# Performance work log

Hardware: AMD Instinct MI355X
Metric: run time of the kernel (lower is better)

## Reference

```python
import jax, jax.numpy as jnp
import numpy as np

B, S, E, H = 4, 1024, 1024, 16
HD = E // H

def setup_inputs() -> dict:
    key = jax.random.key(0)
    ks = jax.random.split(key, 12)
    std = 1.0 / np.sqrt(E)
    inp = {
        "query": jax.random.normal(ks[0], (B, S, E), jnp.float32),
        "key_t": jax.random.normal(ks[1], (B, S, E), jnp.float32),
        "value": jax.random.normal(ks[2], (B, S, E), jnp.float32),
        # causal mask, broadcastable to (B, H, S, S); 0 => masked
        "mask": jnp.tril(jnp.ones((S, S), jnp.int32))[None, None],
        "Wq": jax.random.normal(ks[3], (E, E), jnp.float32) * std,
        "bq": jnp.zeros((E,), jnp.float32),
        "Wk": jax.random.normal(ks[4], (E, E), jnp.float32) * std,
        "bk": jnp.zeros((E,), jnp.float32),
        "Wv": jax.random.normal(ks[5], (E, E), jnp.float32) * std,
        "bv": jnp.zeros((E,), jnp.float32),
        "Wo": jax.random.normal(ks[6], (E, E), jnp.float32) * std,
        "bo": jnp.zeros((E,), jnp.float32),
    }
    return inp

def reference(query, key_t, value, mask, Wq, bq, Wk, bk, Wv, bv, Wo, bo):
    scale = jnp.asarray(np.sqrt(HD), query.dtype)
    # projections (torch Linear: x @ W.T + b), split into heads -> (B, H, S, HD)
    def split_heads(x):
        return x.reshape(B, S, H, HD).transpose(0, 2, 1, 3)
    q = split_heads(query @ Wq.T + bq)
    k = split_heads(key_t @ Wk.T + bk)
    v = split_heads(value @ Wv.T + bv)
    scores = jnp.einsum("bhqd,bhkd->bhqk", q, k) / scale  # (B,H,S,S)
    scores = jnp.where(mask == 0, jnp.asarray(-jnp.inf, scores.dtype), scores)
    attn = jax.nn.softmax(scores, axis=-1)
    # dropout is identity in eval / p=0
    out = jnp.einsum("bhqk,bhkd->bhqd", attn, v)
    out = out.transpose(0, 2, 1, 3).reshape(B, S, E)
    out = out @ Wo.T + bo
    return out, attn
```

## Files before the change

### kernel.cpp

```cpp
#include <hip/hip_runtime.h>
#include <hip/hip_bf16.h>


typedef short bf16x8 __attribute__((ext_vector_type(8)));
typedef float f32x4 __attribute__((ext_vector_type(4)));

__device__ __forceinline__ unsigned short f2bf(float f) {
  union { float f; unsigned u; } v; v.f = f;
  unsigned r = v.u + 0x7FFF + ((v.u >> 16) & 1);
  return (unsigned short)(r >> 16);
}

__device__ __forceinline__ void gload16(const unsigned short* g, unsigned short* l) {
  __builtin_amdgcn_global_load_lds(
      (const __attribute__((address_space(1))) unsigned int*)g,
      (__attribute__((address_space(3))) unsigned int*)l, 16, 0, 0);
}

__global__ __launch_bounds__(256) void cast3_k(
    const float* __restrict__ a, const float* __restrict__ b,
    const float* __restrict__ c,
    unsigned short* __restrict__ oa, unsigned short* __restrict__ ob,
    unsigned short* __restrict__ oc) {
  const float* in = blockIdx.y == 0 ? a : blockIdx.y == 1 ? b : c;
  unsigned short* out = blockIdx.y == 0 ? oa : blockIdx.y == 1 ? ob : oc;
  int i = (blockIdx.x * 256 + threadIdx.x) * 8;
  float4 x = *(const float4*)(in + i);
  float4 y = *(const float4*)(in + i + 4);
  unsigned short t[8] = { f2bf(x.x), f2bf(x.y), f2bf(x.z), f2bf(x.w),
                          f2bf(y.x), f2bf(y.y), f2bf(y.z), f2bf(y.w) };
  *(bf16x8*)(out + i) = *(bf16x8*)t;
}

__global__ __launch_bounds__(256) void cast4_k(
    const float* __restrict__ a, const float* __restrict__ b,
    const float* __restrict__ c, const float* __restrict__ d,
    unsigned short* __restrict__ oa, unsigned short* __restrict__ ob,
    unsigned short* __restrict__ oc, unsigned short* __restrict__ od) {
  const float* in = blockIdx.y == 0 ? a : blockIdx.y == 1 ? b : blockIdx.y == 2 ? c : d;
  unsigned short* out = blockIdx.y == 0 ? oa : blockIdx.y == 1 ? ob : blockIdx.y == 2 ? oc : od;
  int i = (blockIdx.x * 256 + threadIdx.x) * 8;
  float4 x = *(const float4*)(in + i);
  float4 y = *(const float4*)(in + i + 4);
  unsigned short t[8] = { f2bf(x.x), f2bf(x.y), f2bf(x.z), f2bf(x.w),
                          f2bf(y.x), f2bf(y.y), f2bf(y.z), f2bf(y.w) };
  *(bf16x8*)(out + i) = *(bf16x8*)t;
}

__device__ __forceinline__ void gemm_core(
    const unsigned short* __restrict__ A, const unsigned short* __restrict__ W,
    int m0, int n0, int K, unsigned short* As, unsigned short* Bs, f32x4 acc[4][4])
{
  const int tid = threadIdx.x;
  const int w = tid >> 6, lane = tid & 63, quad = lane >> 4, lc = lane & 15;
  const int wm = (w >> 1) * 64, wn = (w & 1) * 64;
  const int lrow = lane >> 3, lg = lane & 7;

  for (int kb = 0; kb < K; kb += 64) {
#pragma unroll
    for (int t = 0; t < 4; t++) {
      int row = w * 32 + t * 8 + lrow;
      int gsw = lg ^ (row & 7);
      gload16(&A[(size_t)(m0 + row) * K + kb + gsw * 8], &As[(w * 32 + t * 8) * 64]);
      gload16(&W[(size_t)(n0 + row) * K + kb + gsw * 8], &Bs[(w * 32 + t * 8) * 64]);
    }
    __syncthreads();
#pragma unroll
    for (int kk = 0; kk < 2; kk++) {
      bf16x8 af[4], bfr[4];
#pragma unroll
      for (int i = 0; i < 4; i++) {
        int ra = wm + i * 16 + lc;
        af[i] = *(const bf16x8*)&As[ra * 64 + (((kk * 4 + quad) ^ (ra & 7)) * 8)];
      }
#pragma unroll
      for (int j = 0; j < 4; j++) {
        int rb = wn + j * 16 + lc;
        bfr[j] = *(const bf16x8*)&Bs[rb * 64 + (((kk * 4 + quad) ^ (rb & 7)) * 8)];
      }
#pragma unroll
      for (int i = 0; i < 4; i++)
#pragma unroll
        for (int j = 0; j < 4; j++)
          acc[i][j] = __builtin_amdgcn_mfma_f32_16x16x32_bf16(af[i], bfr[j], acc[i][j], 0, 0, 0);
    }
    __syncthreads();
  }
}

__global__ __launch_bounds__(256) void gemm_qkv(
    const unsigned short* __restrict__ Xq, const unsigned short* __restrict__ Xk,
    const unsigned short* __restrict__ Xv,
    const unsigned short* __restrict__ Wq, const unsigned short* __restrict__ Wk,
    const unsigned short* __restrict__ Wv,
    const float* __restrict__ bq, const float* __restrict__ bk, const float* __restrict__ bv,
    unsigned short* __restrict__ Qb, unsigned short* __restrict__ Kb,
    unsigned short* __restrict__ Vt)
{
  __shared__ __align__(16) unsigned short S[128 * 136];
  unsigned short* As = S;
  unsigned short* Bs = S + 128 * 64;
  const int z = blockIdx.z;
  const unsigned short* A = z == 0 ? Xq : z == 1 ? Xk : Xv;
  const unsigned short* W = z == 0 ? Wq : z == 1 ? Wk : Wv;
  const float* bias = z == 0 ? bq : z == 1 ? bk : bv;
  unsigned short* outRM = z == 0 ? Qb : Kb;
  const int m0 = blockIdx.x * 128, n0 = blockIdx.y * 128;
  const int tid = threadIdx.x;
  const int w = tid >> 6, lane = tid & 63, quad = lane >> 4, lc = lane & 15;
  const int wm = (w >> 1) * 64, wn = (w & 1) * 64;

  f32x4 acc[4][4] = {};
  gemm_core(A, W, m0, n0, 1024, As, Bs, acc);

  if (z < 2) {
#pragma unroll
    for (int j = 0; j < 4; j++) {
      int col = n0 + wn + j * 16 + lc;
      float bvl = bias[col];
#pragma unroll
      for (int i = 0; i < 4; i++)
#pragma unroll
        for (int r = 0; r < 4; r++) {
          int row = m0 + wm + i * 16 + quad * 4 + r;
          outRM[(size_t)row * 1024 + col] = f2bf(acc[i][j][r] + bvl);
        }
    }
  } else {
    unsigned short* T = S;
#pragma unroll
    for (int j = 0; j < 4; j++) {
      int col = wn + j * 16 + lc;
      float bvl = bias[n0 + col];
#pragma unroll
      for (int i = 0; i < 4; i++)
#pragma unroll
        for (int r = 0; r < 4; r++) {
          int row = wm + i * 16 + quad * 4 + r;
          T[col * 136 + (((row >> 3) ^ (col & 7)) << 3) + (row & 7)] =
              f2bf(acc[i][j][r] + bvl);
        }
    }
    __syncthreads();
    const int b_ = m0 >> 10, sb = m0 & 1023;
#pragma unroll
    for (int it = 0; it < 8; it++) {
      int cl = w * 32 + it * 4 + (lane >> 4);
      int sg = lane & 15;
      int colg = n0 + cl;
      *(bf16x8*)&Vt[((size_t)((b_ * 16 + (colg >> 6)) * 64 + (colg & 63))) * 1024 + sb + sg * 8] =
          *(const bf16x8*)&T[cl * 136 + ((sg ^ (cl & 7)) << 3)];
    }
  }
}

__global__ __launch_bounds__(256) void gemm_out(
    const unsigned short* __restrict__ A, const unsigned short* __restrict__ W,
    const float* __restrict__ bias, float* __restrict__ outf)
{
  __shared__ __align__(16) unsigned short As[128 * 64];
  __shared__ __align__(16) unsigned short Bs[128 * 64];
  const int m0 = blockIdx.x * 128, n0 = blockIdx.y * 128;
  const int tid = threadIdx.x;
  const int w = tid >> 6, lane = tid & 63, quad = lane >> 4, lc = lane & 15;
  const int wm = (w >> 1) * 64, wn = (w & 1) * 64;

  f32x4 acc[4][4] = {};
  gemm_core(A, W, m0, n0, 1024, As, Bs, acc);

#pragma unroll
  for (int j = 0; j < 4; j++) {
    int col = n0 + wn + j * 16 + lc;
    float bvl = bias[col];
#pragma unroll
    for (int i = 0; i < 4; i++)
#pragma unroll
      for (int r = 0; r < 4; r++) {
        int row = m0 + wm + i * 16 + quad * 4 + r;
        outf[(size_t)row * 1024 + col] = acc[i][j][r] + bvl;
      }
  }
}

__global__ __launch_bounds__(256) void attn_fused(
    const unsigned short* __restrict__ Qb,
    const unsigned short* __restrict__ Kb,
    const unsigned short* __restrict__ Vt,
    float* __restrict__ attn,
    unsigned short* __restrict__ O)
{
  __shared__ __align__(16) unsigned short Ks[64 * 64];
  __shared__ __align__(16) unsigned short Vs[64 * 64];
  __shared__ __align__(16) unsigned short Pl[4][16][40];
  __shared__ __align__(16) float          Ps[4][16][36];
  const int bh = blockIdx.x, b = bh >> 4, h = bh & 15;
  const int by = (int)gridDim.y - 1 - (int)blockIdx.y;
  const int q0 = by * 64;
  const int tid = threadIdx.x;
  const int w = tid >> 6, lane = tid & 63, quad = lane >> 4, lc = lane & 15;
  const int g0 = q0 + w * 16;
  const int kt_d = g0 >> 4;
  const int nch = by + 1;
  const int sr = lane >> 3, sg = lane & 7;

  const unsigned short* qp = Qb + ((size_t)(b * 1024 + g0 + lc)) * 1024 + h * 64 + quad * 8;
  bf16x8 a0 = *(const bf16x8*)qp;
  bf16x8 a1 = *(const bf16x8*)(qp + 32);

  float m_[4] = { -1e30f, -1e30f, -1e30f, -1e30f };
  float l_[4] = { 0.f, 0.f, 0.f, 0.f };

  for (int c = 0; c < nch; c++) {
    int kv0 = c * 64;
    {
      int r0 = w * 8 + sr, r1 = 32 + r0;
      gload16(&Kb[((size_t)(b * 1024 + kv0 + r0)) * 1024 + h * 64 + (sg ^ (r0 & 7)) * 8],
              &Ks[(w * 8) * 64]);
      gload16(&Kb[((size_t)(b * 1024 + kv0 + r1)) * 1024 + h * 64 + (sg ^ (r1 & 7)) * 8],
              &Ks[(32 + w * 8) * 64]);
    }
    __syncthreads();
    int tmax = kt_d - c * 4;
    int tlim = tmax < 3 ? tmax : 3;
    for (int t = 0; t <= tlim; t++) {
      int rk = t * 16 + lc;
      const unsigned short* kr = &Ks[rk * 64];
      bf16x8 b0 = *(const bf16x8*)&kr[((quad ^ (rk & 7))) * 8];
      bf16x8 b1 = *(const bf16x8*)&kr[(((quad + 4) ^ (rk & 7))) * 8];
      f32x4 cc = {};
      cc = __builtin_amdgcn_mfma_f32_16x16x32_bf16(a0, b0, cc, 0, 0, 0);
      cc = __builtin_amdgcn_mfma_f32_16x16x32_bf16(a1, b1, cc, 0, 0, 0);
      if (t < tmax) {
#pragma unroll
        for (int r = 0; r < 4; r++) {
          float s = cc[r] * 0.125f;
          float mn = fmaxf(m_[r], s);
          l_[r] = l_[r] * __expf(m_[r] - mn) + __expf(s - mn);
          m_[r] = mn;
        }
      } else {
#pragma unroll
        for (int r = 0; r < 4; r++) {
          int qr = g0 + quad * 4 + r;
          float sv = (kv0 + t * 16 + lc) > qr ? -1e30f : cc[r] * 0.125f;
          float mn = fmaxf(m_[r], sv);
          l_[r] = l_[r] * __expf(m_[r] - mn) + __expf(sv - mn);
          m_[r] = mn;
        }
      }
    }
    __syncthreads();
  }

  float mofs[4];
#pragma unroll
  for (int r = 0; r < 4; r++) {
    float mT = m_[r];
#pragma unroll
    for (int off = 1; off < 16; off <<= 1) mT = fmaxf(mT, __shfl_xor(mT, off));
    float lt = l_[r] * __expf(m_[r] - mT);
#pragma unroll
    for (int off = 1; off < 16; off <<= 1) lt += __shfl_xor(lt, off);
    mofs[r] = mT + __logf(lt);
  }

  float* arow = attn + (size_t)bh * 1024 * 1024;
  f32x4 oacc[4] = {};
  for (int c = 0; c < nch; c++) {
    int kv0 = c * 64;
    {
      int r0 = w * 8 + sr, r1 = 32 + r0;
      gload16(&Kb[((size_t)(b * 1024 + kv0 + r0)) * 1024 + h * 64 + (sg ^ (r0 & 7)) * 8],
              &Ks[(w * 8) * 64]);
      gload16(&Kb[((size_t)(b * 1024 + kv0 + r1)) * 1024 + h * 64 + (sg ^ (r1 & 7)) * 8],
              &Ks[(32 + w * 8) * 64]);
      gload16(&Vt[((size_t)(bh * 64 + r0)) * 1024 + kv0 + (sg ^ (r0 & 7)) * 8],
              &Vs[(w * 8) * 64]);
      gload16(&Vt[((size_t)(bh * 64 + r1)) * 1024 + kv0 + (sg ^ (r1 & 7)) * 8],
              &Vs[(32 + w * 8) * 64]);
    }
    __syncthreads();
    int tmax = kt_d - c * 4;
#pragma unroll
    for (int u = 0; u < 2; u++) {
      if (u * 2 <= tmax) {
#pragma unroll
        for (int t2 = 0; t2 < 2; t2++) {
          int t = u * 2 + t2;
          if (t <= tmax) {
            int rk = t * 16 + lc;
            const unsigned short* kr = &Ks[rk * 64];
            bf16x8 b0 = *(const bf16x8*)&kr[((quad ^ (rk & 7))) * 8];
            bf16x8 b1 = *(const bf16x8*)&kr[(((quad + 4) ^ (rk & 7))) * 8];
            f32x4 cc = {};
            cc = __builtin_amdgcn_mfma_f32_16x16x32_bf16(a0, b0, cc, 0, 0, 0);
            cc = __builtin_amdgcn_mfma_f32_16x16x32_bf16(a1, b1, cc, 0, 0, 0);
#pragma unroll
            for (int r = 0; r < 4; r++) {
              int qr = g0 + quad * 4 + r;
              float p = (kv0 + t * 16 + lc) > qr ? 0.f : __expf(cc[r] * 0.125f - mofs[r]);
              Ps[w][quad * 4 + r][t2 * 16 + lc] = p;
              Pl[w][quad * 4 + r][t2 * 16 + lc] = f2bf(p);
            }
          } else {
#pragma unroll
            for (int r = 0; r < 4; r++) Pl[w][quad * 4 + r][t2 * 16 + lc] = 0;
          }
        }
        bf16x8 pa = *(const bf16x8*)&Pl[w][lc][quad * 8];
#pragma unroll
        for (int j = 0; j < 4; j++) {
          int hd = j * 16 + lc;
          bf16x8 bv = *(const bf16x8*)&Vs[hd * 64 + (((u * 4 + quad) ^ (hd & 7)) * 8)];
          oacc[j] = __builtin_amdgcn_mfma_f32_16x16x32_bf16(pa, bv, oacc[j], 0, 0, 0);
        }
        int nt = tmax - u * 2 + 1; if (nt > 2) nt = 2;
        int srow = lane >> 2, cf = (lane & 3) * 4;
        float* dst = &arow[(size_t)(g0 + srow) * 1024 + kv0 + u * 32];
        *(float4*)(dst + cf) = *(const float4*)&Ps[w][srow][cf];
        if (nt == 2)
          *(float4*)(dst + 16 + cf) = *(const float4*)&Ps[w][srow][16 + cf];
      }
    }
    __syncthreads();
  }

  {
    int rr = lane >> 2, cl = lane & 3;
    float4 z = make_float4(0.f, 0.f, 0.f, 0.f);
    for (int c0 = g0 + 16 + cl * 4; c0 < 1024; c0 += 16)
      *(float4*)&arow[(size_t)(g0 + rr) * 1024 + c0] = z;
  }

  {
    unsigned short* ob = (unsigned short*)&Ps[w][0][0];
#pragma unroll
    for (int j = 0; j < 4; j++)
#pragma unroll
      for (int r = 0; r < 4; r++)
        ob[(quad * 4 + r) * 72 + j * 16 + lc] = f2bf(oacc[j][r]);
#pragma unroll
    for (int it = 0; it < 2; it++) {
      int row = it * 8 + (lane >> 3), off = (lane & 7) * 8;
      *(bf16x8*)&O[((size_t)(b * 1024 + g0 + row)) * 1024 + h * 64 + off] =
          *(const bf16x8*)&ob[row * 72 + off];
    }
  }
}

extern "C" void kernel_launch(void* const* d_in, const int* in_sizes, int n_in,
                              void* d_out, int out_size, void* d_ws, size_t ws_size,
                              hipStream_t stream) {
  const float* query = (const float*)d_in[0];
  const float* key_t = (const float*)d_in[1];
  const float* value = (const float*)d_in[2];
  const float* Wq = (const float*)d_in[4];
  const float* bq = (const float*)d_in[5];
  const float* Wk = (const float*)d_in[6];
  const float* bk = (const float*)d_in[7];
  const float* Wv = (const float*)d_in[8];
  const float* bv = (const float*)d_in[9];
  const float* Wo = (const float*)d_in[10];
  const float* bo = (const float*)d_in[11];

  unsigned short* Xq  = (unsigned short*)d_ws;
  unsigned short* Xk  = Xq  + 4194304;
  unsigned short* Xv  = Xk  + 4194304;
  unsigned short* Wqb = Xv  + 4194304;
  unsigned short* Wkb = Wqb + 1048576;
  unsigned short* Wvb = Wkb + 1048576;
  unsigned short* Wob = Wvb + 1048576;
  unsigned short* Qb  = Wob + 1048576;
  unsigned short* Kb  = Qb  + 4194304;
  unsigned short* Vtb = Kb  + 4194304;
  unsigned short* Ob  = Vtb + 4194304;

  float* outO = (float*)d_out;
  float* attn = outO + 4194304;

  cast3_k<<<dim3(2048, 3), 256, 0, stream>>>(query, key_t, value, Xq, Xk, Xv);
  cast4_k<<<dim3(512, 4), 256, 0, stream>>>(Wq, Wk, Wv, Wo, Wqb, Wkb, Wvb, Wob);

  gemm_qkv<<<dim3(32, 8, 3), 256, 0, stream>>>(Xq, Xk, Xv, Wqb, Wkb, Wvb,
                                               bq, bk, bv, Qb, Kb, Vtb);

  attn_fused<<<dim3(64, 16), 256, 0, stream>>>(Qb, Kb, Vtb, attn, Ob);

  gemm_out<<<dim3(32, 8), 256, 0, stream>>>(Ob, Wob, bo, outO);
}
```

Before: 482.3 us.

## Double-buffer K/V tiles in attention and write attn probabilities from bf16 P

Adds double-buffered K and V shared tiles in both attention passes so the next chunk's global-to-LDS loads are in flight while the current one is computed, with explicit vmcnt waits and raw barriers. Pre-scales Q by 1/8 in bf16 and splits the two MFMA accumulations, so scores no longer need a multiply. Drops the fp32 Ps staging buffer and writes the attn output by widening the bf16 P tile. The attn matrix therefore carries bf16 rounding error, and the hand-placed waitcnt/barrier sequencing is fragile.

Result: no change. 484.3 us (+0.4%).

```diff
diff --git a/kernel.cpp b/kernel.cpp
--- a/kernel.cpp
+++ b/kernel.cpp
@@ -4,11 +4,18 @@
 
 typedef short bf16x8 __attribute__((ext_vector_type(8)));
 typedef float f32x4 __attribute__((ext_vector_type(4)));
+
+#define VMCNT(n) asm volatile("s_waitcnt vmcnt(" #n ")" ::: "memory")
 
 __device__ __forceinline__ unsigned short f2bf(float f) {
   union { float f; unsigned u; } v; v.f = f;
   unsigned r = v.u + 0x7FFF + ((v.u >> 16) & 1);
   return (unsigned short)(r >> 16);
+}
+
+__device__ __forceinline__ float bf2f(unsigned short u) {
+  union { unsigned u; float f; } v; v.u = ((unsigned)u) << 16;
+  return v.f;
 }
 
 __device__ __forceinline__ void gload16(const unsigned short* g, unsigned short* l) {
@@ -189,10 +196,9 @@
     float* __restrict__ attn,
     unsigned short* __restrict__ O)
 {
-  __shared__ __align__(16) unsigned short Ks[64 * 64];
-  __shared__ __align__(16) unsigned short Vs[64 * 64];
+  __shared__ __align__(16) unsigned short Ks[2][64 * 64];
+  __shared__ __align__(16) unsigned short Vs[2][64 * 64];
   __shared__ __align__(16) unsigned short Pl[4][16][40];
-  __shared__ __align__(16) float          Ps[4][16][36];
   const int bh = blockIdx.x, b = bh >> 4, h = bh & 15;
   const int by = (int)gridDim.y - 1 - (int)blockIdx.y;
   const int q0 = by * 64;
@@ -202,38 +208,59 @@
   const int kt_d = g0 >> 4;
   const int nch = by + 1;
   const int sr = lane >> 3, sg = lane & 7;
-
-  const unsigned short* qp = Qb + ((size_t)(b * 1024 + g0 + lc)) * 1024 + h * 64 + quad * 8;
-  bf16x8 a0 = *(const bf16x8*)qp;
-  bf16x8 a1 = *(const bf16x8*)(qp + 32);
+  const int r0_ = w * 8 + sr, r1_ = 32 + r0_;
+
+  bf16x8 a0, a1;
+  {
+    const unsigned short* qp = Qb + ((size_t)(b * 1024 + g0 + lc)) * 1024 + h * 64 + quad * 8;
+    bf16x8 q0v = *(const bf16x8*)qp;
+    bf16x8 q1v = *(const bf16x8*)(qp + 32);
+#pragma unroll
+    for (int i = 0; i < 8; i++) {
+      a0[i] = (short)f2bf(bf2f((unsigned short)q0v[i]) * 0.125f);
+      a1[i] = (short)f2bf(bf2f((unsigned short)q1v[i]) * 0.125f);
+    }
+  }
 
   float m_[4] = { -1e30f, -1e30f, -1e30f, -1e30f };
   float l_[4] = { 0.f, 0.f, 0.f, 0.f };
 
+  {
+    gload16(&Kb[((size_t)(b * 1024 + 0 + r0_)) * 1024 + h * 64 + (sg ^ (r0_ & 7)) * 8],
+            &Ks[0][(w * 8) * 64]);
+    gload16(&Kb[((size_t)(b * 1024 + 0 + r1_)) * 1024 + h * 64 + (sg ^ (r1_ & 7)) * 8],
+            &Ks[0][(32 + w * 8) * 64]);
+  }
   for (int c = 0; c < nch; c++) {
+    const unsigned short* Kc = Ks[c & 1];
     int kv0 = c * 64;
-    {
-      int r0 = w * 8 + sr, r1 = 32 + r0;
-      gload16(&Kb[((size_t)(b * 1024 + kv0 + r0)) * 1024 + h * 64 + (sg ^ (r0 & 7)) * 8],
-              &Ks[(w * 8) * 64]);
-      gload16(&Kb[((size_t)(b * 1024 + kv0 + r1)) * 1024 + h * 64 + (sg ^ (r1 & 7)) * 8],
-              &Ks[(32 + w * 8) * 64]);
-    }
-    __syncthreads();
+    if (c + 1 < nch) {
+      int nv0 = kv0 + 64;
+      unsigned short* Kn = Ks[(c + 1) & 1];
+      gload16(&Kb[((size_t)(b * 1024 + nv0 + r0_)) * 1024 + h * 64 + (sg ^ (r0_ & 7)) * 8],
+              &Kn[(w * 8) * 64]);
+      gload16(&Kb[((size_t)(b * 1024 + nv0 + r1_)) * 1024 + h * 64 + (sg ^ (r1_ & 7)) * 8],
+              &Kn[(32 + w * 8) * 64]);
+      VMCNT(2);
+    } else {
+      VMCNT(0);
+    }
+    __builtin_amdgcn_s_barrier();
+    __builtin_amdgcn_sched_barrier(0);
     int tmax = kt_d - c * 4;
     int tlim = tmax < 3 ? tmax : 3;
     for (int t = 0; t <= tlim; t++) {
       int rk = t * 16 + lc;
-      const unsigned short* kr = &Ks[rk * 64];
+      const unsigned short* kr = &Kc[rk * 64];
       bf16x8 b0 = *(const bf16x8*)&kr[((quad ^ (rk & 7))) * 8];
       bf16x8 b1 = *(const bf16x8*)&kr[(((quad + 4) ^ (rk & 7))) * 8];
-      f32x4 cc = {};
-      cc = __builtin_amdgcn_mfma_f32_16x16x32_bf16(a0, b0, cc, 0, 0, 0);
-      cc = __builtin_amdgcn_mfma_f32_16x16x32_bf16(a1, b1, cc, 0, 0, 0);
+      f32x4 c0 = {}, c1 = {};
+      c0 = __builtin_amdgcn_mfma_f32_16x16x32_bf16(a0, b0, c0, 0, 0, 0);
+      c1 = __builtin_amdgcn_mfma_f32_16x16x32_bf16(a1, b1, c1, 0, 0, 0);
       if (t < tmax) {
 #pragma unroll
         for (int r = 0; r < 4; r++) {
-          float s = cc[r] * 0.125f;
+          float s = c0[r] + c1[r];
           float mn = fmaxf(m_[r], s);
           l_[r] = l_[r] * __expf(m_[r] - mn) + __expf(s - mn);
           m_[r] = mn;
@@ -242,14 +269,16 @@
 #pragma unroll
         for (int r = 0; r < 4; r++) {
           int qr = g0 + quad * 4 + r;
-          float sv = (kv0 + t * 16 + lc) > qr ? -1e30f : cc[r] * 0.125f;
+          float sv = (kv0 + t * 16 + lc) > qr ? -1e30f : c0[r] + c1[r];
           float mn = fmaxf(m_[r], sv);
           l_[r] = l_[r] * __expf(m_[r] - mn) + __expf(sv - mn);
           m_[r] = mn;
         }
       }
     }
-    __syncthreads();
+    asm volatile("s_waitcnt lgkmcnt(0)" ::: "memory");
+    __builtin_amdgcn_s_barrier();
+    __builtin_amdgcn_sched_barrier(0);
   }
 
   float mofs[4];
@@ -266,20 +295,38 @@
 
   float* arow = attn + (size_t)bh * 1024 * 1024;
   f32x4 oacc[4] = {};
+  {
+    gload16(&Kb[((size_t)(b * 1024 + 0 + r0_)) * 1024 + h * 64 + (sg ^ (r0_ & 7)) * 8],
+            &Ks[0][(w * 8) * 64]);
+    gload16(&Kb[((size_t)(b * 1024 + 0 + r1_)) * 1024 + h * 64 + (sg ^ (r1_ & 7)) * 8],
+            &Ks[0][(32 + w * 8) * 64]);
+    gload16(&Vt[((size_t)(bh * 64 + r0_)) * 1024 + 0 + (sg ^ (r0_ & 7)) * 8],
+            &Vs[0][(w * 8) * 64]);
+    gload16(&Vt[((size_t)(bh * 64 + r1_)) * 1024 + 0 + (sg ^ (r1_ & 7)) * 8],
+            &Vs[0][(32 + w * 8) * 64]);
+  }
   for (int c = 0; c < nch; c++) {
+    const unsigned short* Kc = Ks[c & 1];
+    const unsigned short* Vc = Vs[c & 1];
     int kv0 = c * 64;
-    {
-      int r0 = w * 8 + sr, r1 = 32 + r0;
-      gload16(&Kb[((size_t)(b * 1024 + kv0 + r0)) * 1024 + h * 64 + (sg ^ (r0 & 7)) * 8],
-              &Ks[(w * 8) * 64]);
-      gload16(&Kb[((size_t)(b * 1024 + kv0 + r1)) * 1024 + h * 64 + (sg ^ (r1 & 7)) * 8],
-              &Ks[(32 + w * 8) * 64]);
-      gload16(&Vt[((size_t)(bh * 64 + r0)) * 1024 + kv0 + (sg ^ (r0 & 7)) * 8],
-              &Vs[(w * 8) * 64]);
-      gload16(&Vt[((size_t)(bh * 64 + r1)) * 1024 + kv0 + (sg ^ (r1 & 7)) * 8],
-              &Vs[(32 + w * 8) * 64]);
-    }
-    __syncthreads();
+    if (c + 1 < nch) {
+      int nv0 = kv0 + 64;
+      unsigned short* Kn = Ks[(c + 1) & 1];
+      unsigned short* Vn = Vs[(c + 1) & 1];
+      gload16(&Kb[((size_t)(b * 1024 + nv0 + r0_)) * 1024 + h * 64 + (sg ^ (r0_ & 7)) * 8],
+              &Kn[(w * 8) * 64]);
+      gload16(&Kb[((size_t)(b * 1024 + nv0 + r1_)) * 1024 + h * 64 + (sg ^ (r1_ & 7)) * 8],
+              &Kn[(32 + w * 8) * 64]);
+      gload16(&Vt[((size_t)(bh * 64 + r0_)) * 1024 + nv0 + (sg ^ (r0_ & 7)) * 8],
+              &Vn[(w * 8) * 64]);
+      gload16(&Vt[((size_t)(bh * 64 + r1_)) * 1024 + nv0 + (sg ^ (r1_ & 7)) * 8],
+              &Vn[(32 + w * 8) * 64]);
+      VMCNT(4);
+    } else {
+      VMCNT(0);
+    }
+    __builtin_amdgcn_s_barrier();
+    __builtin_amdgcn_sched_barrier(0);
     int tmax = kt_d - c * 4;
 #pragma unroll
     for (int u = 0; u < 2; u++) {
@@ -289,17 +336,17 @@
           int t = u * 2 + t2;
           if (t <= tmax) {
             int rk = t * 16 + lc;
-            const unsigned short* kr = &Ks[rk * 64];
+            const unsigned short* kr = &Kc[rk * 64];
             bf16x8 b0 = *(const bf16x8*)&kr[((quad ^ (rk & 7))) * 8];
             bf16x8 b1 = *(const bf16x8*)&kr[(((quad + 4) ^ (rk & 7))) * 8];
-            f32x4 cc = {};
-            cc = __builtin_amdgcn_mfma_f32_16x16x32_bf16(a0, b0, cc, 0, 0, 0);
-            cc = __builtin_amdgcn_mfma_f32_16x16x32_bf16(a1, b1, cc, 0, 0, 0);
+            f32x4 c0 = {}, c1 = {};
+            c0 = __builtin_amdgcn_mfma_f32_16x16x32_bf16(a0, b0, c0, 0, 0, 0);
+            c1 = __builtin_amdgcn_mfma_f32_16x16x32_bf16(a1, b1, c1, 0, 0, 0);
 #pragma unroll
             for (int r = 0; r < 4; r++) {
               int qr = g0 + quad * 4 + r;
-              float p = (kv0 + t * 16 + lc) > qr ? 0.f : __expf(cc[r] * 0.125f - mofs[r]);
-              Ps[w][quad * 4 + r][t2 * 16 + lc] = p;
+              float p = (kv0 + t * 16 + lc) > qr ? 0.f
+                        : __expf(c0[r] + c1[r] - mofs[r]);
               Pl[w][quad * 4 + r][t2 * 16 + lc] = f2bf(p);
             }
           } else {
@@ -307,22 +354,30 @@
             for (int r = 0; r < 4; r++) Pl[w][quad * 4 + r][t2 * 16 + lc] = 0;
           }
         }
+        {
+          int srow = lane >> 2, c4 = lane & 3;
+          bf16x8 pv8 = *(const bf16x8*)&Pl[w][srow][c4 * 8];
+          float4 f0, f1;
+          f0.x = bf2f((unsigned short)pv8[0]); f0.y = bf2f((unsigned short)pv8[1]);
+          f0.z = bf2f((unsigned short)pv8[2]); f0.w = bf2f((unsigned short)pv8[3]);
+          f1.x = bf2f((unsigned short)pv8[4]); f1.y = bf2f((unsigned short)pv8[5]);
+          f1.z = bf2f((unsigned short)pv8[6]); f1.w = bf2f((unsigned short)pv8[7]);
+          float* dst = &arow[(size_t)(g0 + srow) * 1024 + kv0 + u * 32 + c4 * 8];
+          *(float4*)dst = f0;
+          *(float4*)(dst + 4) = f1;
+        }
         bf16x8 pa = *(const bf16x8*)&Pl[w][lc][quad * 8];
 #pragma unroll
         for (int j = 0; j < 4; j++) {
           int hd = j * 16 + lc;
-          bf16x8 bv = *(const bf16x8*)&Vs[hd * 64 + (((u * 4 + quad) ^ (hd & 7)) * 8)];
+          bf16x8 bv = *(const bf16x8*)&Vc[hd * 64 + (((u * 4 + quad) ^ (hd & 7)) * 8)];
           oacc[j] = __builtin_amdgcn_mfma_f32_16x16x32_bf16(pa, bv, oacc[j], 0, 0, 0);
         }
-        int nt = tmax - u * 2 + 1; if (nt > 2) nt = 2;
-        int srow = lane >> 2, cf = (lane & 3) * 4;
-        float* dst = &arow[(size_t)(g0 + srow) * 1024 + kv0 + u * 32];
-        *(float4*)(dst + cf) = *(const float4*)&Ps[w][srow][cf];
-        if (nt == 2)
-          *(float4*)(dst + 16 + cf) = *(const float4*)&Ps[w][srow][16 + cf];
       }
     }
-    __syncthreads();
+    asm volatile("s_waitcnt lgkmcnt(0)" ::: "memory");
+    __builtin_amdgcn_s_barrier();
+    __builtin_amdgcn_sched_barrier(0);
   }
 
   {
@@ -333,7 +388,7 @@
   }
 
   {
-    unsigned short* ob = (unsigned short*)&Ps[w][0][0];
+    unsigned short* ob = &Ks[0][0] + w * 1152;
 #pragma unroll
     for (int j = 0; j < 4; j++)
 #pragma unroll
```
